# Optimization experiments

Hardware: AMD Instinct MI355X
Metric: run time of the kernel (lower is better)

## Reference

```python
import jax, jax.numpy as jnp
import numpy as np

NUM_HEADS = 4
CATEGORY_SIZE = 128
NUM_TOKENS = 64


def setup_inputs() -> dict:
    key = jax.random.key(0)
    k1, k2, k3 = jax.random.split(key, 3)
    b, n, c = 2, 65536, 192
    qkv = jax.random.normal(k1, (b, n, 3 * c), dtype=jnp.float32)
    sim = jax.random.normal(k2, (b, n, NUM_TOKENS), dtype=jnp.float32)
    proj_w = jax.random.normal(k3, (c, c), dtype=jnp.float32) * 0.02  # nn.Linear weight (out, in)
    proj_b = jnp.zeros((c,), dtype=jnp.float32)
    logit_scale = jnp.log(10.0) * jnp.ones((1, 1), dtype=jnp.float32)
    return {"qkv": qkv, "sim": sim, "proj_w": proj_w, "proj_b": proj_b,
            "logit_scale": logit_scale, "H": 256, "W": 256}


def reference(qkv, sim, proj_w, proj_b, logit_scale, H, W):
    b, n, c3 = qkv.shape
    c = c3 // 3
    hd = c // NUM_HEADS
    gs = min(n, CATEGORY_SIZE)
    ng = (n + gs - 1) // gs
    pad_n = ng * gs - n

    # cluster id per token, sort tokens by cluster (dynamic reorder)
    tk_id = jnp.argmax(sim, axis=-1)                    # (b, n) int
    sort_idx = jnp.argsort(tk_id, axis=-1)              # permutation
    rev_idx = jnp.argsort(sort_idx, axis=-1)            # inverse permutation (index_reverse)

    shuffled = jnp.take_along_axis(qkv, sort_idx[..., None], axis=1)  # (b, n, 3c)
    if pad_n > 0:
        pad = shuffled[:, n - pad_n:n][:, ::-1]         # torch.flip of tail
        shuffled = jnp.concatenate([shuffled, pad], axis=1)

    # (b, ng, gs, 3, nh, hd) -> (3, b, ng, nh, gs, hd)
    y = shuffled.reshape(b, ng, gs, 3, NUM_HEADS, hd)
    qkv_g = jnp.transpose(y, (3, 0, 1, 4, 2, 5))
    q, k, v = qkv_g[0], qkv_g[1], qkv_g[2]

    # clamped learned logit scale (no normalization in original code)
    scale = jnp.exp(jnp.minimum(logit_scale, jnp.log(1.0 / 0.01)))[0, 0]
    attn = jnp.einsum('bgnsd,bgntd->bgnst', q, k) * scale   # (b, ng, nh, gs, gs)
    attn = jax.nn.softmax(attn, axis=-1)
    out = jnp.einsum('bgnst,bgntd->bgnsd', attn, v)         # (b, ng, nh, gs, hd)

    out = jnp.transpose(out, (0, 1, 3, 2, 4)).reshape(b, ng * gs, c)[:, :n]
    x = jnp.take_along_axis(out, rev_idx[..., None], axis=1)  # unshuffle
    x = x @ proj_w.T + proj_b
    return x
```

## Files before the change

kernel.cpp:

```cpp
#include <hip/hip_runtime.h>

#define B_  2
#define N_  65536
#define C_  192
#define NH_ 4
#define HD_ 48
#define GS_ 128
#define NG_ 512
#define NTILES_ 256

typedef __attribute__((ext_vector_type(8))) short short8;
typedef __attribute__((ext_vector_type(4))) short short4v;
typedef __attribute__((ext_vector_type(4))) float f32x4;

__device__ __forceinline__ unsigned short f2bf(float f) {
    unsigned u = __float_as_uint(f);
    unsigned r = (u + 0x7FFFu + ((u >> 16) & 1u)) >> 16;
    return (unsigned short)r;
}
__device__ __forceinline__ float bf2f(unsigned short s) {
    return __uint_as_float(((unsigned)s) << 16);
}
__device__ __forceinline__ unsigned cvt_pk(float a, float b) {
    unsigned r;
    asm("v_cvt_pk_bf16_f32 %0, %1, %2" : "=v"(r) : "v"(a), "v"(b));
    return r;
}

#if defined(__has_builtin)
#if __has_builtin(__builtin_amdgcn_mfma_f32_16x16x16bf16_1k)
#define HAVE_MFMA16_1K 1
#endif
#endif
__device__ __forceinline__ f32x4 mfma16(short4v a, short4v b, f32x4 c) {
#ifdef HAVE_MFMA16_1K
    return __builtin_amdgcn_mfma_f32_16x16x16bf16_1k(a, b, c, 0, 0, 0);
#else
    f32x4 d;
    asm volatile("v_mfma_f32_16x16x16_bf16 %0, %1, %2, %3"
                 : "=&v"(d) : "v"(a), "v"(b), "v"(c));
    return d;
#endif
}

__global__ __launch_bounds__(256) void argmax_kernel(const float* __restrict__ sim,
                                                     int* __restrict__ keys) {
    int lane  = threadIdx.x & 63;
    int token = blockIdx.x * 4 + (threadIdx.x >> 6);
    float v = sim[(size_t)token * 64 + lane];
    int idx = lane;
    #pragma unroll
    for (int m = 1; m < 64; m <<= 1) {
        float ov = __shfl_xor(v, m);
        int   oi = __shfl_xor(idx, m);
        if (ov > v || (ov == v && oi < idx)) { v = ov; idx = oi; }
    }
    if (lane == 0) keys[token] = idx;
}

__global__ __launch_bounds__(256) void hist_kernel(const int* __restrict__ keys,
                                                   int* __restrict__ counts) {
    __shared__ int hcnt[64];
    int tid  = threadIdx.x;
    int tile = blockIdx.x & (NTILES_ - 1);
    int bz   = blockIdx.x >> 8;
    if (tid < 64) hcnt[tid] = 0;
    __syncthreads();
    int k = keys[bz * N_ + tile * 256 + tid];
    atomicAdd(&hcnt[k], 1);
    __syncthreads();
    if (tid < 64) counts[(bz * NTILES_ + tile) * 64 + tid] = hcnt[tid];
}

__global__ __launch_bounds__(256) void scan_kernel(int* __restrict__ counts) {
    __shared__ int qsum[4][64];
    __shared__ int kbase[64];
    int bz = blockIdx.x;
    int k  = threadIdx.x & 63;
    int qt = threadIdx.x >> 6;
    int base_idx = (bz * NTILES_) * 64 + k;

    int sum = 0;
    #pragma unroll 8
    for (int t = qt * 64; t < qt * 64 + 64; ++t) sum += counts[base_idx + t * 64];
    qsum[qt][k] = sum;
    __syncthreads();

    if (qt == 0) {
        int tot = qsum[0][k] + qsum[1][k] + qsum[2][k] + qsum[3][k];
        int incl = tot;
        #pragma unroll
        for (int off = 1; off < 64; off <<= 1) {
            int v = __shfl_up(incl, off);
            if (k >= off) incl += v;
        }
        kbase[k] = incl - tot;
    }
    __syncthreads();

    int run = kbase[k];
    for (int q2 = 0; q2 < qt; ++q2) run += qsum[q2][k];
    #pragma unroll 8
    for (int t = qt * 64; t < qt * 64 + 64; ++t) {
        int idx = base_idx + t * 64;
        int c = counts[idx];
        counts[idx] = run;
        run += c;
    }
}

__global__ __launch_bounds__(256) void rank_kernel(const int* __restrict__ keys,
                                                   const int* __restrict__ counts,
                                                   int* __restrict__ sidx) {
    __shared__ int whist[4 * 64];
    int tid  = threadIdx.x;
    int tile = blockIdx.x & (NTILES_ - 1);
    int bz   = blockIdx.x >> 8;
    whist[tid] = 0;
    __syncthreads();

    int tok = tile * 256 + tid;
    int key = keys[bz * N_ + tok];
    int w = tid >> 6, lane = tid & 63;

    unsigned long long mask = ~0ull;
    #pragma unroll
    for (int b = 0; b < 6; ++b) {
        unsigned long long bb = __ballot((key >> b) & 1);
        mask &= ((key >> b) & 1) ? bb : ~bb;
    }
    unsigned long long lt = (lane == 0) ? 0ull : (~0ull >> (64 - lane));
    int rank = __popcll(mask & lt);
    if (rank == 0) whist[w * 64 + key] = __popcll(mask);
    __syncthreads();

    int base = counts[(bz * NTILES_ + tile) * 64 + key];
    for (int w2 = 0; w2 < w; ++w2) base += whist[w2 * 64 + key];
    int pos = base + rank;
    sidx[bz * N_ + pos] = tok;
}

#define KP_STRIDE 104
#define VT_STRIDE 132
#define KP_BYTES  (128 * KP_STRIDE * 2)
#define VT_BYTES  (48 * VT_STRIDE * 2)
#define SM_SIZE   (KP_BYTES + VT_BYTES + 512)

__global__ __launch_bounds__(256, 4) void attn_kernel(const float* __restrict__ qkv,
                                                      const float* __restrict__ lscale,
                                                      const int* __restrict__ sort_idx,
                                                      unsigned short* __restrict__ oattn) {
    __shared__ __align__(16) char smem[SM_SIZE];
    unsigned short* kp = (unsigned short*)smem;
    unsigned short* vt = (unsigned short*)(smem + KP_BYTES);
    int* sidx_s = (int*)(smem + KP_BYTES + VT_BYTES);

    int x  = blockIdx.x;
    int gg = (x & 7) | ((x >> 5) << 3);
    int h  = (x >> 3) & 3;
    int g  = gg & (NG_ - 1);
    int bz = gg >> 9;
    int tid = threadIdx.x;

    if (tid < 128) sidx_s[tid] = sort_idx[bz * N_ + g * GS_ + tid];
    __syncthreads();

    int lane = tid & 63, wid = tid >> 6;
    int lr = lane & 15, lg = lane >> 4;
    int qt0 = wid * 2, qt1 = qt0 + 1;
    float scale = __expf(fminf(lscale[0], 4.60517019f));

    int r0s = lg * 8;
    int r1s = 16 + lg * 8;
    int r2s = (lg < 2) ? 32 + lg * 8 : (lg - 2) * 8;
    const float* q0p = qkv + (size_t)(bz * N_ + sidx_s[qt0 * 16 + lr]) * 576 + h * 48;
    const float* q1p = qkv + (size_t)(bz * N_ + sidx_s[qt1 * 16 + lr]) * 576 + h * 48;
    float4 qA0 = *(const float4*)(q0p + r0s), qA1 = *(const float4*)(q0p + r0s + 4);
    float4 qB0 = *(const float4*)(q0p + r1s), qB1 = *(const float4*)(q0p + r1s + 4);
    float4 qC0 = *(const float4*)(q0p + r2s), qC1 = *(const float4*)(q0p + r2s + 4);
    float4 pA0 = *(const float4*)(q1p + r0s), pA1 = *(const float4*)(q1p + r0s + 4);
    float4 pB0 = *(const float4*)(q1p + r1s), pB1 = *(const float4*)(q1p + r1s + 4);
    float4 pC0 = *(const float4*)(q1p + r2s), pC1 = *(const float4*)(q1p + r2s + 4);

    #pragma unroll
    for (int it = 0; it < 6; ++it) {
        int f = it * 256 + tid;
        int row = f / 12, piece = f - row * 12;
        float4 kf = *(const float4*)(qkv + (size_t)(bz * N_ + sidx_s[row]) * 576 + 192 + h * 48 + piece * 4);
        unsigned h01 = cvt_pk(kf.x, kf.y), h23 = cvt_pk(kf.z, kf.w);
        float hx = __uint_as_float(h01 << 16), hy = __uint_as_float(h01 & 0xFFFF0000u);
        float hz = __uint_as_float(h23 << 16), hw = __uint_as_float(h23 & 0xFFFF0000u);
        unsigned l01 = cvt_pk(kf.x - hx, kf.y - hy), l23 = cvt_pk(kf.z - hz, kf.w - hw);
        *(uint2*)(kp + row * KP_STRIDE + piece * 4)      = make_uint2(h01, h23);
        *(uint2*)(kp + row * KP_STRIDE + 48 + piece * 4) = make_uint2(l01, l23);
    }
    #pragma unroll
    for (int it = 0; it < 6; ++it) {
        int f = it * 256 + tid;
        int row = f / 12, piece = f - row * 12;
        float4 vf = *(const float4*)(qkv + (size_t)(bz * N_ + sidx_s[row]) * 576 + 384 + h * 48 + piece * 4);
        int d = piece * 4;
        vt[(d + 0) * VT_STRIDE + row] = f2bf(vf.x);
        vt[(d + 1) * VT_STRIDE + row] = f2bf(vf.y);
        vt[(d + 2) * VT_STRIDE + row] = f2bf(vf.z);
        vt[(d + 3) * VT_STRIDE + row] = f2bf(vf.w);
    }

    unsigned af0[5][4], af1[5][4];
    {
        float a0[8] = {qA0.x,qA0.y,qA0.z,qA0.w,qA1.x,qA1.y,qA1.z,qA1.w};
        float b0[8] = {qB0.x,qB0.y,qB0.z,qB0.w,qB1.x,qB1.y,qB1.z,qB1.w};
        float c0[8] = {qC0.x,qC0.y,qC0.z,qC0.w,qC1.x,qC1.y,qC1.z,qC1.w};
        float a1[8] = {pA0.x,pA0.y,pA0.z,pA0.w,pA1.x,pA1.y,pA1.z,pA1.w};
        float b1[8] = {pB0.x,pB0.y,pB0.z,pB0.w,pB1.x,pB1.y,pB1.z,pB1.w};
        float c1[8] = {pC0.x,pC0.y,pC0.z,pC0.w,pC1.x,pC1.y,pC1.z,pC1.w};
        #pragma unroll
        for (int j = 0; j < 8; ++j) {
            a0[j] *= scale; b0[j] *= scale; c0[j] *= scale;
            a1[j] *= scale; b1[j] *= scale; c1[j] *= scale;
        }
        #pragma unroll
        for (int w = 0; w < 4; ++w) {
            af0[0][w] = cvt_pk(a0[2*w], a0[2*w+1]);
            af1[0][w] = cvt_pk(a1[2*w], a1[2*w+1]);
            af0[3][w] = af0[0][w];
            af1[3][w] = af1[0][w];
            {
                unsigned t0 = cvt_pk(b0[2*w], b0[2*w+1]);
                float hx = __uint_as_float(t0 << 16), hy = __uint_as_float(t0 & 0xFFFF0000u);
                af0[2][w] = cvt_pk(b0[2*w] - hx, b0[2*w+1] - hy);
                unsigned t1 = cvt_pk(b1[2*w], b1[2*w+1]);
                float ix = __uint_as_float(t1 << 16), iy = __uint_as_float(t1 & 0xFFFF0000u);
                af1[2][w] = cvt_pk(b1[2*w] - ix, b1[2*w+1] - iy);
            }
            if (lg < 2) {
                af0[1][w] = cvt_pk(c0[2*w], c0[2*w+1]);
                af1[1][w] = cvt_pk(c1[2*w], c1[2*w+1]);
                af0[4][w] = af0[1][w];
                af1[4][w] = af1[1][w];
            } else {
                unsigned t0 = cvt_pk(c0[2*w], c0[2*w+1]);
                float hx = __uint_as_float(t0 << 16), hy = __uint_as_float(t0 & 0xFFFF0000u);
                af0[1][w] = cvt_pk(c0[2*w] - hx, c0[2*w+1] - hy);
                unsigned t1 = cvt_pk(c1[2*w], c1[2*w+1]);
                float ix = __uint_as_float(t1 << 16), iy = __uint_as_float(t1 & 0xFFFF0000u);
                af1[1][w] = cvt_pk(c1[2*w] - ix, c1[2*w+1] - iy);
                af0[4][w] = 0; af1[4][w] = 0;
            }
        }
    }
    __syncthreads();

    const int boffs[5] = { lg * 8, (32 + lg * 8) % 48, 16 + lg * 8,
                           48 + lg * 8, (lg < 2) ? 80 + lg * 8 : 48 };
    f32x4 acc0[8], acc1[8];
    #pragma unroll
    for (int kt = 0; kt < 8; ++kt) { acc0[kt] = (f32x4)0.f; acc1[kt] = (f32x4)0.f; }

    #pragma unroll
    for (int s = 0; s < 5; ++s) {
        union { short8 v; unsigned u[4]; } ua, ub;
        #pragma unroll
        for (int w = 0; w < 4; ++w) { ua.u[w] = af0[s][w]; ub.u[w] = af1[s][w]; }
        short8 b0 = ua.v, b1 = ub.v;
        #pragma unroll
        for (int kt = 0; kt < 8; ++kt) {
            short8 a = *(const short8*)(kp + (size_t)(kt * 16 + lr) * KP_STRIDE + boffs[s]);
            acc0[kt] = __builtin_amdgcn_mfma_f32_16x16x32_bf16(a, b0, acc0[kt], 0, 0, 0);
            acc1[kt] = __builtin_amdgcn_mfma_f32_16x16x32_bf16(a, b1, acc1[kt], 0, 0, 0);
        }
    }

    short4v pf0[8], pf1[8];
    {
        float m0v = -1e30f, m1v = -1e30f;
        #pragma unroll
        for (int kt = 0; kt < 8; ++kt)
            #pragma unroll
            for (int r = 0; r < 4; ++r) {
                m0v = fmaxf(m0v, acc0[kt][r]);
                m1v = fmaxf(m1v, acc1[kt][r]);
            }
        m0v = fmaxf(m0v, __shfl_xor(m0v, 16)); m0v = fmaxf(m0v, __shfl_xor(m0v, 32));
        m1v = fmaxf(m1v, __shfl_xor(m1v, 16)); m1v = fmaxf(m1v, __shfl_xor(m1v, 32));
        float s0v = 0.f, s1v = 0.f;
        #pragma unroll
        for (int kt = 0; kt < 8; ++kt)
            #pragma unroll
            for (int r = 0; r < 4; ++r) {
                float e0 = __expf(acc0[kt][r] - m0v);
                float e1 = __expf(acc1[kt][r] - m1v);
                acc0[kt][r] = e0; acc1[kt][r] = e1;
                s0v += e0; s1v += e1;
            }
        s0v += __shfl_xor(s0v, 16); s0v += __shfl_xor(s0v, 32);
        s1v += __shfl_xor(s1v, 16); s1v += __shfl_xor(s1v, 32);
        float inv0 = 1.f / s0v, inv1 = 1.f / s1v;
        #pragma unroll
        for (int kt = 0; kt < 8; ++kt) {
            union { short4v v; unsigned u[2]; } u0, u1;
            u0.u[0] = cvt_pk(acc0[kt][0] * inv0, acc0[kt][1] * inv0);
            u0.u[1] = cvt_pk(acc0[kt][2] * inv0, acc0[kt][3] * inv0);
            u1.u[0] = cvt_pk(acc1[kt][0] * inv1, acc1[kt][1] * inv1);
            u1.u[1] = cvt_pk(acc1[kt][2] * inv1, acc1[kt][3] * inv1);
            pf0[kt] = u0.v; pf1[kt] = u1.v;
        }
    }

    f32x4 o0[3], o1[3];
    #pragma unroll
    for (int dt = 0; dt < 3; ++dt) { o0[dt] = (f32x4)0.f; o1[dt] = (f32x4)0.f; }
    #pragma unroll
    for (int kt = 0; kt < 8; ++kt) {
        #pragma unroll
        for (int dt = 0; dt < 3; ++dt) {
            short4v vf = *(const short4v*)(vt + (size_t)(dt * 16 + lr) * VT_STRIDE + kt * 16 + lg * 4);
            o0[dt] = mfma16(pf0[kt], vf, o0[dt]);
            o1[dt] = mfma16(pf1[kt], vf, o1[dt]);
        }
    }

    #pragma unroll
    for (int dt = 0; dt < 3; ++dt)
        #pragma unroll
        for (int r = 0; r < 4; ++r) {
            int row0 = qt0 * 16 + lg * 4 + r;
            int row1 = qt1 * 16 + lg * 4 + r;
            oattn[(size_t)(bz * N_ + g * GS_ + row0) * C_ + h * HD_ + dt * 16 + lr] = f2bf(o0[dt][r]);
            oattn[(size_t)(bz * N_ + g * GS_ + row1) * C_ + h * HD_ + dt * 16 + lr] = f2bf(o1[dt][r]);
        }
}

__global__ __launch_bounds__(256) void wconv_kernel(const float* __restrict__ W,
                                                    unsigned short* __restrict__ wbf) {
    int i = blockIdx.x * 256 + threadIdx.x;
    float4 f = ((const float4*)W)[i];
    uint2 p;
    p.x = (unsigned)f2bf(f.x) | ((unsigned)f2bf(f.y) << 16);
    p.y = (unsigned)f2bf(f.z) | ((unsigned)f2bf(f.w) << 16);
    ((uint2*)wbf)[i] = p;
}

__global__ __launch_bounds__(256) void proj2_kernel(const unsigned short* __restrict__ oattn,
                                                    const int* __restrict__ sidx,
                                                    const unsigned short* __restrict__ wbf,
                                                    const float* __restrict__ bias,
                                                    float* __restrict__ out) {
    __shared__ int mout[128];
    int tid = threadIdx.x;
    int s0  = blockIdx.x * 128;

    if (tid < 128) {
        int s = s0 + tid;
        int bz = s >> 16;
        mout[tid] = bz * N_ + sidx[s];
    }
    __syncthreads();

    int lane = tid & 63, wid = tid >> 6;
    int lr = lane & 15, lg = lane >> 4;
    int mt0 = wid * 2, mt1 = wid * 2 + 1;

    const unsigned short* xr0 = oattn + (size_t)(s0 + mt0 * 16 + lr) * C_ + lg * 8;
    const unsigned short* xr1 = oattn + (size_t)(s0 + mt1 * 16 + lr) * C_ + lg * 8;
    const unsigned short* wr  = wbf + (size_t)lr * C_ + lg * 8;

    f32x4 acc[2][12];
    #pragma unroll
    for (int mt = 0; mt < 2; ++mt)
        #pragma unroll
        for (int jt = 0; jt < 12; ++jt) acc[mt][jt] = (f32x4)0.f;

    #pragma unroll
    for (int ks = 0; ks < 6; ++ks) {
        short8 a0 = *(const short8*)(xr0 + ks * 32);
        short8 a1 = *(const short8*)(xr1 + ks * 32);
        #pragma unroll
        for (int jt = 0; jt < 12; ++jt) {
            short8 b = *(const short8*)(wr + (size_t)jt * 16 * C_ + ks * 32);
            acc[0][jt] = __builtin_amdgcn_mfma_f32_16x16x32_bf16(a0, b, acc[0][jt], 0, 0, 0);
            acc[1][jt] = __builtin_amdgcn_mfma_f32_16x16x32_bf16(a1, b, acc[1][jt], 0, 0, 0);
        }
    }

    #pragma unroll
    for (int jt = 0; jt < 12; ++jt) {
        int j = jt * 16 + lr;
        float bj = bias[j];
        #pragma unroll
        for (int r = 0; r < 4; ++r) {
            int row0 = mout[mt0 * 16 + lg * 4 + r];
            int row1 = mout[mt1 * 16 + lg * 4 + r];
            out[(size_t)row0 * C_ + j] = acc[0][jt][r] + bj;
            out[(size_t)row1 * C_ + j] = acc[1][jt][r] + bj;
        }
    }
}

extern "C" void kernel_launch(void* const* d_in, const int* in_sizes, int n_in,
                              void* d_out, int out_size, void* d_ws, size_t ws_size,
                              hipStream_t stream) {
    const float* qkv    = (const float*)d_in[0];
    const float* sim    = (const float*)d_in[1];
    const float* proj_w = (const float*)d_in[2];
    const float* proj_b = (const float*)d_in[3];
    const float* lscale = (const float*)d_in[4];
    float* out = (float*)d_out;

    char* ws = (char*)d_ws;
    int* keys   = (int*)(ws);
    int* sidx   = (int*)(ws + 1048576);
    int* counts = (int*)(ws + 1572864);
    unsigned short* oattn = (unsigned short*)(ws + 1703936);
    unsigned short* wbf   = (unsigned short*)(ws + 1703936 + 50331648);

    argmax_kernel<<<32768, 256, 0, stream>>>(sim, keys);
    hist_kernel<<<B_ * NTILES_, 256, 0, stream>>>(keys, counts);
    scan_kernel<<<B_, 256, 0, stream>>>(counts);
    rank_kernel<<<B_ * NTILES_, 256, 0, stream>>>(keys, counts, sidx);
    wconv_kernel<<<36, 256, 0, stream>>>(proj_w, wbf);
    attn_kernel<<<B_ * NG_ * NH_, 256, 0, stream>>>(qkv, lscale, sidx, oattn);
    proj2_kernel<<<(B_ * N_) / 128, 256, 0, stream>>>(oattn, sidx, wbf, proj_b, out);
}
```

Measured before the change: 218.7 us.

## Process all four heads per attention block with full-row gathered loads

The attention kernel now runs one 512-thread block per group, covering all four heads, instead of one 256-thread block per (group, head). Each gathered token row is read as contiguous 768-byte Q and K/V spans, so gathers are coalesced and there are fewer index indirections. Q is staged through LDS as split hi/lo bf16 and then loaded into registers, and each wave handles four query tiles in two passes. LDS use grows to about 156 KB of dynamic shared memory, which cuts occupancy and leaves fewer, larger blocks.

```diff
diff --git a/kernel.cpp b/kernel.cpp
--- a/kernel.cpp
+++ b/kernel.cpp
@@ -18,14 +18,13 @@
     unsigned r = (u + 0x7FFFu + ((u >> 16) & 1u)) >> 16;
     return (unsigned short)r;
 }
-__device__ __forceinline__ float bf2f(unsigned short s) {
-    return __uint_as_float(((unsigned)s) << 16);
-}
 __device__ __forceinline__ unsigned cvt_pk(float a, float b) {
     unsigned r;
     asm("v_cvt_pk_bf16_f32 %0, %1, %2" : "=v"(r) : "v"(a), "v"(b));
     return r;
 }
+__device__ __forceinline__ float lo16f(unsigned u) { return __uint_as_float(u << 16); }
+__device__ __forceinline__ float hi16f(unsigned u) { return __uint_as_float(u & 0xFFFF0000u); }
 
 #if defined(__has_builtin)
 #if __has_builtin(__builtin_amdgcn_mfma_f32_16x16x16bf16_1k)
@@ -140,195 +139,175 @@
     sidx[bz * N_ + pos] = tok;
 }
 
-#define KP_STRIDE 104
+#define KQ_STRIDE 104
 #define VT_STRIDE 132
-#define KP_BYTES  (128 * KP_STRIDE * 2)
-#define VT_BYTES  (48 * VT_STRIDE * 2)
-#define SM_SIZE   (KP_BYTES + VT_BYTES + 512)
-
-__global__ __launch_bounds__(256, 4) void attn_kernel(const float* __restrict__ qkv,
+#define KQ_HEAD   (128 * KQ_STRIDE)
+#define KQ_BYTES  (4 * KQ_HEAD * 2)
+#define VT_HEAD   (48 * VT_STRIDE)
+#define VT_BYTES  (4 * VT_HEAD * 2)
+#define SM_SIZE   (KQ_BYTES + VT_BYTES + 512)
+
+__global__ __launch_bounds__(512, 2) void attn_kernel(const float* __restrict__ qkv,
                                                       const float* __restrict__ lscale,
                                                       const int* __restrict__ sort_idx,
                                                       unsigned short* __restrict__ oattn) {
-    __shared__ __align__(16) char smem[SM_SIZE];
-    unsigned short* kp = (unsigned short*)smem;
-    unsigned short* vt = (unsigned short*)(smem + KP_BYTES);
-    int* sidx_s = (int*)(smem + KP_BYTES + VT_BYTES);
-
-    int x  = blockIdx.x;
-    int gg = (x & 7) | ((x >> 5) << 3);
-    int h  = (x >> 3) & 3;
-    int g  = gg & (NG_ - 1);
-    int bz = gg >> 9;
+    extern __shared__ __align__(16) char smem[];
+    unsigned short* kq = (unsigned short*)smem;
+    unsigned short* vt = (unsigned short*)(smem + KQ_BYTES);
+    int* sidx_s = (int*)(smem + KQ_BYTES + VT_BYTES);
+
+    int g  = blockIdx.x & (NG_ - 1);
+    int bz = blockIdx.x >> 9;
     int tid = threadIdx.x;
-
     if (tid < 128) sidx_s[tid] = sort_idx[bz * N_ + g * GS_ + tid];
+    __syncthreads();
+
+    float scale = __expf(fminf(lscale[0], 4.60517019f));
+
+    #pragma unroll 6
+    for (int it = 0; it < 12; ++it) {
+        int f = it * 512 + tid;
+        int row = f / 48, p = f - row * 48;
+        int h = p / 12, dk = 4 * (p - h * 12);
+        float4 q4 = *(const float4*)(qkv + (size_t)(bz * N_ + sidx_s[row]) * 576 + p * 4);
+        q4.x *= scale; q4.y *= scale; q4.z *= scale; q4.w *= scale;
+        unsigned h01 = cvt_pk(q4.x, q4.y), h23 = cvt_pk(q4.z, q4.w);
+        unsigned l01 = cvt_pk(q4.x - lo16f(h01), q4.y - hi16f(h01));
+        unsigned l23 = cvt_pk(q4.z - lo16f(h23), q4.w - hi16f(h23));
+        unsigned short* dst = kq + h * KQ_HEAD + row * KQ_STRIDE + dk;
+        *(uint2*)dst        = make_uint2(h01, h23);
+        *(uint2*)(dst + 48) = make_uint2(l01, l23);
+    }
     __syncthreads();
 
     int lane = tid & 63, wid = tid >> 6;
     int lr = lane & 15, lg = lane >> 4;
-    int qt0 = wid * 2, qt1 = qt0 + 1;
-    float scale = __expf(fminf(lscale[0], 4.60517019f));
-
-    int r0s = lg * 8;
-    int r1s = 16 + lg * 8;
-    int r2s = (lg < 2) ? 32 + lg * 8 : (lg - 2) * 8;
-    const float* q0p = qkv + (size_t)(bz * N_ + sidx_s[qt0 * 16 + lr]) * 576 + h * 48;
-    const float* q1p = qkv + (size_t)(bz * N_ + sidx_s[qt1 * 16 + lr]) * 576 + h * 48;
-    float4 qA0 = *(const float4*)(q0p + r0s), qA1 = *(const float4*)(q0p + r0s + 4);
-    float4 qB0 = *(const float4*)(q0p + r1s), qB1 = *(const float4*)(q0p + r1s + 4);
-    float4 qC0 = *(const float4*)(q0p + r2s), qC1 = *(const float4*)(q0p + r2s + 4);
-    float4 pA0 = *(const float4*)(q1p + r0s), pA1 = *(const float4*)(q1p + r0s + 4);
-    float4 pB0 = *(const float4*)(q1p + r1s), pB1 = *(const float4*)(q1p + r1s + 4);
-    float4 pC0 = *(const float4*)(q1p + r2s), pC1 = *(const float4*)(q1p + r2s + 4);
-
-    #pragma unroll
-    for (int it = 0; it < 6; ++it) {
-        int f = it * 256 + tid;
-        int row = f / 12, piece = f - row * 12;
-        float4 kf = *(const float4*)(qkv + (size_t)(bz * N_ + sidx_s[row]) * 576 + 192 + h * 48 + piece * 4);
-        unsigned h01 = cvt_pk(kf.x, kf.y), h23 = cvt_pk(kf.z, kf.w);
-        float hx = __uint_as_float(h01 << 16), hy = __uint_as_float(h01 & 0xFFFF0000u);
-        float hz = __uint_as_float(h23 << 16), hw = __uint_as_float(h23 & 0xFFFF0000u);
-        unsigned l01 = cvt_pk(kf.x - hx, kf.y - hy), l23 = cvt_pk(kf.z - hz, kf.w - hw);
-        *(uint2*)(kp + row * KP_STRIDE + piece * 4)      = make_uint2(h01, h23);
-        *(uint2*)(kp + row * KP_STRIDE + 48 + piece * 4) = make_uint2(l01, l23);
-    }
-    #pragma unroll
-    for (int it = 0; it < 6; ++it) {
-        int f = it * 256 + tid;
-        int row = f / 12, piece = f - row * 12;
-        float4 vf = *(const float4*)(qkv + (size_t)(bz * N_ + sidx_s[row]) * 576 + 384 + h * 48 + piece * 4);
-        int d = piece * 4;
-        vt[(d + 0) * VT_STRIDE + row] = f2bf(vf.x);
-        vt[(d + 1) * VT_STRIDE + row] = f2bf(vf.y);
-        vt[(d + 2) * VT_STRIDE + row] = f2bf(vf.z);
-        vt[(d + 3) * VT_STRIDE + row] = f2bf(vf.w);
-    }
-
-    unsigned af0[5][4], af1[5][4];
-    {
-        float a0[8] = {qA0.x,qA0.y,qA0.z,qA0.w,qA1.x,qA1.y,qA1.z,qA1.w};
-        float b0[8] = {qB0.x,qB0.y,qB0.z,qB0.w,qB1.x,qB1.y,qB1.z,qB1.w};
-        float c0[8] = {qC0.x,qC0.y,qC0.z,qC0.w,qC1.x,qC1.y,qC1.z,qC1.w};
-        float a1[8] = {pA0.x,pA0.y,pA0.z,pA0.w,pA1.x,pA1.y,pA1.z,pA1.w};
-        float b1[8] = {pB0.x,pB0.y,pB0.z,pB0.w,pB1.x,pB1.y,pB1.z,pB1.w};
-        float c1[8] = {pC0.x,pC0.y,pC0.z,pC0.w,pC1.x,pC1.y,pC1.z,pC1.w};
-        #pragma unroll
-        for (int j = 0; j < 8; ++j) {
-            a0[j] *= scale; b0[j] *= scale; c0[j] *= scale;
-            a1[j] *= scale; b1[j] *= scale; c1[j] *= scale;
-        }
-        #pragma unroll
-        for (int w = 0; w < 4; ++w) {
-            af0[0][w] = cvt_pk(a0[2*w], a0[2*w+1]);
-            af1[0][w] = cvt_pk(a1[2*w], a1[2*w+1]);
-            af0[3][w] = af0[0][w];
-            af1[3][w] = af1[0][w];
-            {
-                unsigned t0 = cvt_pk(b0[2*w], b0[2*w+1]);
-                float hx = __uint_as_float(t0 << 16), hy = __uint_as_float(t0 & 0xFFFF0000u);
-                af0[2][w] = cvt_pk(b0[2*w] - hx, b0[2*w+1] - hy);
-                unsigned t1 = cvt_pk(b1[2*w], b1[2*w+1]);
-                float ix = __uint_as_float(t1 << 16), iy = __uint_as_float(t1 & 0xFFFF0000u);
-                af1[2][w] = cvt_pk(b1[2*w] - ix, b1[2*w+1] - iy);
-            }
-            if (lg < 2) {
-                af0[1][w] = cvt_pk(c0[2*w], c0[2*w+1]);
-                af1[1][w] = cvt_pk(c1[2*w], c1[2*w+1]);
-                af0[4][w] = af0[1][w];
-                af1[4][w] = af1[1][w];
-            } else {
-                unsigned t0 = cvt_pk(c0[2*w], c0[2*w+1]);
-                float hx = __uint_as_float(t0 << 16), hy = __uint_as_float(t0 & 0xFFFF0000u);
-                af0[1][w] = cvt_pk(c0[2*w] - hx, c0[2*w+1] - hy);
-                unsigned t1 = cvt_pk(c1[2*w], c1[2*w+1]);
-                float ix = __uint_as_float(t1 << 16), iy = __uint_as_float(t1 & 0xFFFF0000u);
-                af1[1][w] = cvt_pk(c1[2*w] - ix, c1[2*w+1] - iy);
-                af0[4][w] = 0; af1[4][w] = 0;
-            }
+    int hh = wid >> 1, half = wid & 1;
+    const unsigned short* qbase = kq + hh * KQ_HEAD;
+    short8 qf[4][3];
+    int qo1 = (lg < 2) ? (32 + lg * 8) : (48 + (lg - 2) * 8);
+    #pragma unroll
+    for (int j = 0; j < 4; ++j) {
+        const unsigned short* qr = qbase + ((half * 4 + j) * 16 + lr) * KQ_STRIDE;
+        qf[j][0] = *(const short8*)(qr + lg * 8);
+        qf[j][1] = *(const short8*)(qr + qo1);
+        qf[j][2] = *(const short8*)(qr + 64 + lg * 8);
+    }
+    __syncthreads();
+
+    #pragma unroll 8
+    for (int it = 0; it < 24; ++it) {
+        int f = it * 512 + tid;
+        int row = f / 96, p = f - row * 96;
+        float4 v4 = *(const float4*)(qkv + (size_t)(bz * N_ + sidx_s[row]) * 576 + 192 + p * 4);
+        if (p < 48) {
+            int h = p / 12, dk = 4 * (p - h * 12);
+            unsigned h01 = cvt_pk(v4.x, v4.y), h23 = cvt_pk(v4.z, v4.w);
+            unsigned l01 = cvt_pk(v4.x - lo16f(h01), v4.y - hi16f(h01));
+            unsigned l23 = cvt_pk(v4.z - lo16f(h23), v4.w - hi16f(h23));
+            unsigned short* dst = kq + h * KQ_HEAD + row * KQ_STRIDE + dk;
+            *(uint2*)dst        = make_uint2(h01, h23);
+            *(uint2*)(dst + 48) = make_uint2(l01, l23);
+        } else {
+            int p2 = p - 48;
+            int h = p2 / 12, d0 = 4 * (p2 - h * 12);
+            unsigned short* vd = vt + h * VT_HEAD + row;
+            vd[(d0 + 0) * VT_STRIDE] = f2bf(v4.x);
+            vd[(d0 + 1) * VT_STRIDE] = f2bf(v4.y);
+            vd[(d0 + 2) * VT_STRIDE] = f2bf(v4.z);
+            vd[(d0 + 3) * VT_STRIDE] = f2bf(v4.w);
         }
     }
     __syncthreads();
 
     const int boffs[5] = { lg * 8, (32 + lg * 8) % 48, 16 + lg * 8,
                            48 + lg * 8, (lg < 2) ? 80 + lg * 8 : 48 };
-    f32x4 acc0[8], acc1[8];
-    #pragma unroll
-    for (int kt = 0; kt < 8; ++kt) { acc0[kt] = (f32x4)0.f; acc1[kt] = (f32x4)0.f; }
-
-    #pragma unroll
-    for (int s = 0; s < 5; ++s) {
-        union { short8 v; unsigned u[4]; } ua, ub;
-        #pragma unroll
-        for (int w = 0; w < 4; ++w) { ua.u[w] = af0[s][w]; ub.u[w] = af1[s][w]; }
-        short8 b0 = ua.v, b1 = ub.v;
+    const unsigned short* kb = kq + hh * KQ_HEAD;
+    const unsigned short* vb = vt + hh * VT_HEAD;
+
+    #pragma unroll
+    for (int pass = 0; pass < 2; ++pass) {
+        int j0 = pass * 2, j1 = j0 + 1;
+        int qt0 = half * 4 + j0, qt1 = qt0 + 1;
+
+        f32x4 acc0[8], acc1[8];
+        #pragma unroll
+        for (int kt = 0; kt < 8; ++kt) { acc0[kt] = (f32x4)0.f; acc1[kt] = (f32x4)0.f; }
+
+        #pragma unroll
+        for (int s = 0; s < 5; ++s) {
+            short8 b0, b1;
+            if (s < 3)       { b0 = qf[j0][s]; b1 = qf[j1][s]; }
+            else if (s == 3) { b0 = qf[j0][0]; b1 = qf[j1][0]; }
+            else             { b0 = (lg < 2) ? qf[j0][1] : (short8)0;
+                               b1 = (lg < 2) ? qf[j1][1] : (short8)0; }
+            #pragma unroll
+            for (int kt = 0; kt < 8; ++kt) {
+                short8 a = *(const short8*)(kb + (size_t)(kt * 16 + lr) * KQ_STRIDE + boffs[s]);
+                acc0[kt] = __builtin_amdgcn_mfma_f32_16x16x32_bf16(a, b0, acc0[kt], 0, 0, 0);
+                acc1[kt] = __builtin_amdgcn_mfma_f32_16x16x32_bf16(a, b1, acc1[kt], 0, 0, 0);
+            }
+        }
+
+        short4v pf0[8], pf1[8];
+        {
+            float m0v = -1e30f, m1v = -1e30f;
+            #pragma unroll
+            for (int kt = 0; kt < 8; ++kt)
+                #pragma unroll
+                for (int r = 0; r < 4; ++r) {
+                    m0v = fmaxf(m0v, acc0[kt][r]);
+                    m1v = fmaxf(m1v, acc1[kt][r]);
+                }
+            m0v = fmaxf(m0v, __shfl_xor(m0v, 16)); m0v = fmaxf(m0v, __shfl_xor(m0v, 32));
+            m1v = fmaxf(m1v, __shfl_xor(m1v, 16)); m1v = fmaxf(m1v, __shfl_xor(m1v, 32));
+            float s0v = 0.f, s1v = 0.f;
+            #pragma unroll
+            for (int kt = 0; kt < 8; ++kt)
+                #pragma unroll
+                for (int r = 0; r < 4; ++r) {
+                    float e0 = __expf(acc0[kt][r] - m0v);
+                    float e1 = __expf(acc1[kt][r] - m1v);
+                    acc0[kt][r] = e0; acc1[kt][r] = e1;
+                    s0v += e0; s1v += e1;
+                }
+            s0v += __shfl_xor(s0v, 16); s0v += __shfl_xor(s0v, 32);
+            s1v += __shfl_xor(s1v, 16); s1v += __shfl_xor(s1v, 32);
+            float inv0 = 1.f / s0v, inv1 = 1.f / s1v;
+            #pragma unroll
+            for (int kt = 0; kt < 8; ++kt) {
+                union { short4v v; unsigned u[2]; } u0, u1;
+                u0.u[0] = cvt_pk(acc0[kt][0] * inv0, acc0[kt][1] * inv0);
+                u0.u[1] = cvt_pk(acc0[kt][2] * inv0, acc0[kt][3] * inv0);
+                u1.u[0] = cvt_pk(acc1[kt][0] * inv1, acc1[kt][1] * inv1);
+                u1.u[1] = cvt_pk(acc1[kt][2] * inv1, acc1[kt][3] * inv1);
+                pf0[kt] = u0.v; pf1[kt] = u1.v;
+            }
+        }
+
+        f32x4 o0[3], o1[3];
+        #pragma unroll
+        for (int dt = 0; dt < 3; ++dt) { o0[dt] = (f32x4)0.f; o1[dt] = (f32x4)0.f; }
         #pragma unroll
         for (int kt = 0; kt < 8; ++kt) {
-            short8 a = *(const short8*)(kp + (size_t)(kt * 16 + lr) * KP_STRIDE + boffs[s]);
-            acc0[kt] = __builtin_amdgcn_mfma_f32_16x16x32_bf16(a, b0, acc0[kt], 0, 0, 0);
-            acc1[kt] = __builtin_amdgcn_mfma_f32_16x16x32_bf16(a, b1, acc1[kt], 0, 0, 0);
-        }
-    }
-
-    short4v pf0[8], pf1[8];
-    {
-        float m0v = -1e30f, m1v = -1e30f;
-        #pragma unroll
-        for (int kt = 0; kt < 8; ++kt)
+            #pragma unroll
+            for (int dt = 0; dt < 3; ++dt) {
+                short4v vf = *(const short4v*)(vb + (size_t)(dt * 16 + lr) * VT_STRIDE + kt * 16 + lg * 4);
+                o0[dt] = mfma16(pf0[kt], vf, o0[dt]);
+                o1[dt] = mfma16(pf1[kt], vf, o1[dt]);
+            }
+        }
+
+        #pragma unroll
+        for (int dt = 0; dt < 3; ++dt)
             #pragma unroll
             for (int r = 0; r < 4; ++r) {
-                m0v = fmaxf(m0v, acc0[kt][r]);
-                m1v = fmaxf(m1v, acc1[kt][r]);
+                int row0 = qt0 * 16 + lg * 4 + r;
+                int row1 = qt1 * 16 + lg * 4 + r;
+                oattn[(size_t)(bz * N_ + g * GS_ + row0) * C_ + hh * HD_ + dt * 16 + lr] = f2bf(o0[dt][r]);
+                oattn[(size_t)(bz * N_ + g * GS_ + row1) * C_ + hh * HD_ + dt * 16 + lr] = f2bf(o1[dt][r]);
             }
-        m0v = fmaxf(m0v, __shfl_xor(m0v, 16)); m0v = fmaxf(m0v, __shfl_xor(m0v, 32));
-        m1v = fmaxf(m1v, __shfl_xor(m1v, 16)); m1v = fmaxf(m1v, __shfl_xor(m1v, 32));
-        float s0v = 0.f, s1v = 0.f;
-        #pragma unroll
-        for (int kt = 0; kt < 8; ++kt)
-            #pragma unroll
-            for (int r = 0; r < 4; ++r) {
-                float e0 = __expf(acc0[kt][r] - m0v);
-                float e1 = __expf(acc1[kt][r] - m1v);
-                acc0[kt][r] = e0; acc1[kt][r] = e1;
-                s0v += e0; s1v += e1;
-            }
-        s0v += __shfl_xor(s0v, 16); s0v += __shfl_xor(s0v, 32);
-        s1v += __shfl_xor(s1v, 16); s1v += __shfl_xor(s1v, 32);
-        float inv0 = 1.f / s0v, inv1 = 1.f / s1v;
-        #pragma unroll
-        for (int kt = 0; kt < 8; ++kt) {
-            union { short4v v; unsigned u[2]; } u0, u1;
-            u0.u[0] = cvt_pk(acc0[kt][0] * inv0, acc0[kt][1] * inv0);
-            u0.u[1] = cvt_pk(acc0[kt][2] * inv0, acc0[kt][3] * inv0);
-            u1.u[0] = cvt_pk(acc1[kt][0] * inv1, acc1[kt][1] * inv1);
-            u1.u[1] = cvt_pk(acc1[kt][2] * inv1, acc1[kt][3] * inv1);
-            pf0[kt] = u0.v; pf1[kt] = u1.v;
-        }
-    }
-
-    f32x4 o0[3], o1[3];
-    #pragma unroll
-    for (int dt = 0; dt < 3; ++dt) { o0[dt] = (f32x4)0.f; o1[dt] = (f32x4)0.f; }
-    #pragma unroll
-    for (int kt = 0; kt < 8; ++kt) {
-        #pragma unroll
-        for (int dt = 0; dt < 3; ++dt) {
-            short4v vf = *(const short4v*)(vt + (size_t)(dt * 16 + lr) * VT_STRIDE + kt * 16 + lg * 4);
-            o0[dt] = mfma16(pf0[kt], vf, o0[dt]);
-            o1[dt] = mfma16(pf1[kt], vf, o1[dt]);
-        }
-    }
-
-    #pragma unroll
-    for (int dt = 0; dt < 3; ++dt)
-        #pragma unroll
-        for (int r = 0; r < 4; ++r) {
-            int row0 = qt0 * 16 + lg * 4 + r;
-            int row1 = qt1 * 16 + lg * 4 + r;
-            oattn[(size_t)(bz * N_ + g * GS_ + row0) * C_ + h * HD_ + dt * 16 + lr] = f2bf(o0[dt][r]);
-            oattn[(size_t)(bz * N_ + g * GS_ + row1) * C_ + h * HD_ + dt * 16 + lr] = f2bf(o1[dt][r]);
-        }
+    }
 }
 
 __global__ __launch_bounds__(256) void wconv_kernel(const float* __restrict__ W,
@@ -414,11 +393,15 @@
     unsigned short* oattn = (unsigned short*)(ws + 1703936);
     unsigned short* wbf   = (unsigned short*)(ws + 1703936 + 50331648);
 
+    static_assert(SM_SIZE <= 163840, "LDS over 160K");
+    (void)hipFuncSetAttribute((const void*)attn_kernel,
+                              hipFuncAttributeMaxDynamicSharedMemorySize, SM_SIZE);
+
     argmax_kernel<<<32768, 256, 0, stream>>>(sim, keys);
     hist_kernel<<<B_ * NTILES_, 256, 0, stream>>>(keys, counts);
     scan_kernel<<<B_, 256, 0, stream>>>(counts);
     rank_kernel<<<B_ * NTILES_, 256, 0, stream>>>(keys, counts, sidx);
     wconv_kernel<<<36, 256, 0, stream>>>(proj_w, wbf);
-    attn_kernel<<<B_ * NG_ * NH_, 256, 0, stream>>>(qkv, lscale, sidx, oattn);
+    attn_kernel<<<B_ * NG_, 512, SM_SIZE, stream>>>(qkv, lscale, sidx, oattn);
     proj2_kernel<<<(B_ * N_) / 128, 256, 0, stream>>>(oattn, sidx, wbf, proj_b, out);
 }
```

Measured after the change: 257.1 us. 17.6% more time.
